# Kernel optimization log

Measured on AMD Instinct MI355X. Metric: run time of the kernel, lower is better.

The kernel has to match this reference:

```python
import jax, jax.numpy as jnp
import numpy as np

D_MODEL = 1024
N_HEADS = 16
HEAD_DIM = D_MODEL // N_HEADS


def setup_inputs() -> dict:
    key = jax.random.key(0)
    k_x, k_qkv, k_out = jax.random.split(key, 3)
    x = jax.random.normal(k_x, (4, 2048, D_MODEL), dtype=jnp.float32)
    # nn.Linear weights are (out_features, in_features); init std=0.02
    w_qkv = jax.random.normal(k_qkv, (3 * D_MODEL, D_MODEL), dtype=jnp.float32) * 0.02
    w_out = jax.random.normal(k_out, (D_MODEL, D_MODEL), dtype=jnp.float32) * 0.02
    return {"x": x, "w_qkv": w_qkv, "w_out": w_out}


def reference(x, w_qkv, w_out):
    B, T, C = x.shape
    H, Dh = N_HEADS, HEAD_DIM
    # qkv projection: x @ w_qkv.T -> (B, T, 3C)
    qkv = jnp.einsum('btc,oc->bto', x, w_qkv)
    q, k, v = jnp.split(qkv, 3, axis=-1)

    def split_heads(t):
        return t.reshape(B, T, H, Dh).transpose(0, 2, 1, 3)  # (B, H, T, Dh)

    q, k, v = split_heads(q), split_heads(k), split_heads(v)
    scale = jnp.sqrt(jnp.asarray(Dh, dtype=x.dtype))
    scores = jnp.einsum('bhqd,bhkd->bhqk', q, k) / scale  # (B, H, T, T)
    causal = jnp.tril(jnp.ones((T, T), dtype=bool))
    scores = jnp.where(causal[None, None], scores, jnp.asarray(-jnp.inf, dtype=scores.dtype))
    attn = jax.nn.softmax(scores, axis=-1)
    out = jnp.einsum('bhqk,bhkd->bhqd', attn, v)  # (B, H, T, Dh)
    out = out.transpose(0, 2, 1, 3).reshape(B, T, C)
    return jnp.einsum('btc,oc->bto', out, w_out)
```

## Files before the change

kernel.cpp:

```cpp
#include <hip/hip_runtime.h>

typedef __attribute__((ext_vector_type(8))) short bf16x8;
typedef __attribute__((ext_vector_type(4))) float f32x4;
typedef __attribute__((ext_vector_type(16))) float f32x16;
typedef __attribute__((ext_vector_type(4))) int i32x4;
using u16 = unsigned short;

constexpr int Bsz = 4, T = 2048, C = 1024, H = 16, Dh = 64;
constexpr int Mrows = Bsz * T;
constexpr int K_DIM = 1024;
constexpr float QSCALE = 0.18033688011112042f;

__device__ inline u16 f2bf(float f) {
    unsigned u = __builtin_bit_cast(unsigned, f);
    u += 0x7FFFu + ((u >> 16) & 1u);
    return (u16)(u >> 16);
}

__device__ inline void g2l16(const void* g, void* l) {
    __builtin_amdgcn_global_load_lds((const __attribute__((address_space(1))) void*)g,
                                     (__attribute__((address_space(3))) void*)l, 16, 0, 0);
}

__device__ inline unsigned pk2(float lo, float hi) {
    unsigned d;
    asm("v_cvt_pk_bf16_f32 %0, %1, %2" : "=v"(d) : "v"(lo), "v"(hi));
    return d;
}
__device__ inline void swap32(unsigned& a, unsigned& b) {
    asm("v_permlane32_swap_b32 %0, %1" : "+v"(a), "+v"(b));
}

__global__ __launch_bounds__(256)
void cvt_k(const float* __restrict__ x, const float* __restrict__ wq,
           const float* __restrict__ wo, u16* __restrict__ xb,
           u16* __restrict__ wqb, u16* __restrict__ wob)
{
    int idx = blockIdx.x * 256 + threadIdx.x;
    const float* src; u16* dst; int rel;
    if (idx < 1048576)      { src = x;  dst = xb;  rel = idx; }
    else if (idx < 1441792) { src = wq; dst = wqb; rel = idx - 1048576; }
    else                    { src = wo; dst = wob; rel = idx - 1441792; }
    size_t off = (size_t)rel * 8;
    float4 a = *(const float4*)(src + off);
    float4 b = *(const float4*)(src + off + 4);
    unsigned r0 = (unsigned)f2bf(a.x) | ((unsigned)f2bf(a.y) << 16);
    unsigned r1 = (unsigned)f2bf(a.z) | ((unsigned)f2bf(a.w) << 16);
    unsigned r2 = (unsigned)f2bf(b.x) | ((unsigned)f2bf(b.y) << 16);
    unsigned r3 = (unsigned)f2bf(b.z) | ((unsigned)f2bf(b.w) << 16);
    *(uint4*)(dst + off) = make_uint4(r0, r1, r2, r3);
}

__device__ inline void stage_g(u16* lds, const u16* gb, int ldg, int tid) {
    #pragma unroll
    for (int i = 0; i < 4; ++i) {
        int ch = i * 256 + tid;
        int r = ch >> 3, c8 = ch & 7;
        int sc = c8 ^ (r & 7);
        g2l16(gb + (size_t)r * ldg + sc * 8, lds + (i * 256 + (tid & 192)) * 8);
    }
}

template<int MODE>
__global__ __launch_bounds__(256)
void gemm_k(const u16* __restrict__ Ab, const u16* __restrict__ Bb,
            float* __restrict__ Op, u16* __restrict__ qws,
            u16* __restrict__ kws, u16* __restrict__ vtws)
{
    __shared__ alignas(16) u16 As[128 * 64];
    __shared__ alignas(16) u16 Bs[128 * 64];
    const int tid = threadIdx.x;
    const int l = tid & 63, wid = tid >> 6;
    const int wm = wid >> 1, wn = wid & 1;
    const int lane16 = l & 15, lhi = l >> 4;
    const int m0 = blockIdx.x * 128;
    const int n0 = (MODE == 2 ? 2 * C : 0) + blockIdx.y * 128;

    const u16* Abase = Ab + (size_t)m0 * K_DIM;
    const u16* Bbase = Bb + (size_t)n0 * K_DIM;

    f32x4 acc[4][4] = {};

    for (int ks = 0; ks < K_DIM / 64; ++ks) {
        __syncthreads();
        stage_g(As, Abase + ks * 64, K_DIM, tid);
        stage_g(Bs, Bbase + ks * 64, K_DIM, tid);
        __syncthreads();
        #pragma unroll
        for (int kc = 0; kc < 2; kc++) {
            bf16x8 af[4], bfr[4];
            #pragma unroll
            for (int mi = 0; mi < 4; mi++) {
                int row = wm * 64 + mi * 16 + lane16;
                int byte = row * 128 + kc * 64 + lhi * 16; byte ^= (row & 7) << 4;
                af[mi] = *(const bf16x8*)((const char*)As + byte);
            }
            #pragma unroll
            for (int ni = 0; ni < 4; ni++) {
                int row = wn * 64 + ni * 16 + lane16;
                int byte = row * 128 + kc * 64 + lhi * 16; byte ^= (row & 7) << 4;
                bfr[ni] = *(const bf16x8*)((const char*)Bs + byte);
            }
            #pragma unroll
            for (int mi = 0; mi < 4; mi++)
                #pragma unroll
                for (int ni = 0; ni < 4; ni++) {
                    if constexpr (MODE == 2)
                        acc[mi][ni] = __builtin_amdgcn_mfma_f32_16x16x32_bf16(
                            bfr[ni], af[mi], acc[mi][ni], 0, 0, 0);
                    else
                        acc[mi][ni] = __builtin_amdgcn_mfma_f32_16x16x32_bf16(
                            af[mi], bfr[ni], acc[mi][ni], 0, 0, 0);
                }
        }
    }

    if constexpr (MODE == 2) {
        #pragma unroll
        for (int mi = 0; mi < 4; mi++)
            #pragma unroll
            for (int ni = 0; ni < 4; ni++)
                #pragma unroll
                for (int r = 0; r < 4; r++) {
                    int wr = n0 + wn * 64 + ni * 16 + lhi * 4 + r;
                    int tg = m0 + wm * 64 + mi * 16 + lane16;
                    int hh = (wr >> 6) & 15, d = wr & 63;
                    int bb = tg >> 11, tt = tg & 2047;
                    size_t off = (((size_t)bb * H + hh) * Dh + d) * T + tt;
                    vtws[off] = f2bf(acc[mi][ni][r]);
                }
    } else {
        #pragma unroll
        for (int mi = 0; mi < 4; mi++)
            #pragma unroll
            for (int ni = 0; ni < 4; ni++)
                #pragma unroll
                for (int r = 0; r < 4; r++) {
                    int gm = m0 + wm * 64 + mi * 16 + lhi * 4 + r;
                    int gn = n0 + wn * 64 + ni * 16 + lane16;
                    float val = acc[mi][ni][r];
                    if constexpr (MODE == 0) {
                        int hh = (gn >> 6) & 15, d = gn & 63;
                        int bb = gm >> 11, t = gm & 2047;
                        size_t off = (((size_t)bb * H + hh) * T + t) * Dh + d;
                        if (gn < C) qws[off] = f2bf(val * QSCALE);
                        else        kws[off] = f2bf(val);
                    } else {
                        Op[(size_t)gm * C + gn] = val;
                    }
                }
    }
}

__device__ inline bf16x8 ldsfrag(const u16* base, int row, int cc) {
    int byte = (row << 7) + (cc << 4); byte ^= (row & 7) << 4;
    return *(const bf16x8*)((const char*)base + byte);
}

__device__ inline void stage_t(u16* lds, const u16* gb, int rstride, int tid) {
    #pragma unroll
    for (int it = 0; it < 2; ++it) {
        int chunk = it * 256 + tid;
        int r = chunk >> 3, cc = chunk & 7;
        int sc = cc ^ (r & 7);
        g2l16(gb + (size_t)r * rstride + sc * 8, lds + (it * 256 + (tid & 192)) * 8);
    }
}

__global__ __launch_bounds__(256, 2)
void attn_k(const u16* __restrict__ qws, const u16* __restrict__ kws,
            const u16* __restrict__ vtws, u16* __restrict__ ows)
{
    __shared__ alignas(16) u16 KL[2][64 * 64];
    __shared__ alignas(16) u16 VL[2][64 * 64];

    const int bid = blockIdx.x;
    const int qt   = (bid < 256) ? 7 - (bid & 7) : (bid & 7);
    const int head = ((bid < 256) ? 0 : 32) + ((bid & 255) >> 3);
    const int b = head >> 4, h = head & 15;
    const int tid = threadIdx.x, w = tid >> 6, l = tid & 63;
    const int l31 = l & 31, hi = l >> 5;

    const size_t hoff = (size_t)head * (T * Dh);
    const u16* Qg  = qws + hoff;
    const u16* Kg  = kws + hoff;
    const u16* Vtg = vtws + hoff;

    const int qb_w = qt * 256 + w * 64;
    const int nt = 4 * qt + 4;

    bf16x8 qf[2][4];
    #pragma unroll
    for (int q2 = 0; q2 < 2; ++q2)
        #pragma unroll
        for (int c = 0; c < 4; ++c)
            qf[q2][c] = *(const bf16x8*)(Qg + (size_t)(qb_w + q2 * 32 + l31) * Dh
                                         + c * 16 + hi * 8);

    f32x16 o[2][2] = {};
    float mrun[2] = {-__builtin_inff(), -__builtin_inff()};
    float lrun[2] = {0.f, 0.f};

    stage_t(KL[0], Kg, Dh, tid);
    stage_t(VL[0], Vtg, T, tid);
    __syncthreads();

    for (int t = 0; t < nt; ++t) {
        const int cur = t & 1;
        if (t + 1 < nt) {
            stage_t(KL[cur ^ 1], Kg + (size_t)(t + 1) * 64 * Dh, Dh, tid);
            stage_t(VL[cur ^ 1], Vtg + (t + 1) * 64, T, tid);
        }
        const int kv0 = t * 64;
        if (kv0 <= qb_w + 63) {
            const u16* Kb = KL[cur];
            const u16* Vb = VL[cur];

            bf16x8 kf[2][4];
            #pragma unroll
            for (int kvh = 0; kvh < 2; ++kvh)
                #pragma unroll
                for (int c = 0; c < 4; ++c)
                    kf[kvh][c] = ldsfrag(Kb, kvh * 32 + l31, c * 2 + hi);

            unsigned paf[2][4][4];
            const bool act0 = kv0 <= qb_w + 31;

            #pragma unroll
            for (int q2 = 0; q2 < 2; ++q2) {
                if (q2 == 0 && !act0) continue;
                f32x16 s0{}, s1{};
                #pragma unroll
                for (int c = 0; c < 4; ++c) {
                    s0 = __builtin_amdgcn_mfma_f32_32x32x16_bf16(kf[0][c], qf[q2][c], s0, 0, 0, 0);
                    s1 = __builtin_amdgcn_mfma_f32_32x32x16_bf16(kf[1][c], qf[q2][c], s1, 0, 0, 0);
                }
                const int qbb = qb_w + q2 * 32;
                if (kv0 + 63 > qbb) {
                    int qg = qbb + l31;
                    #pragma unroll
                    for (int r = 0; r < 16; ++r) {
                        int kvg = kv0 + (r & 3) + 8 * (r >> 2) + 4 * hi;
                        if (kvg > qg)      s0[r] = -__builtin_inff();
                        if (kvg + 32 > qg) s1[r] = -__builtin_inff();
                    }
                }
                float pmax = s0[0];
                #pragma unroll
                for (int r = 1; r < 16; ++r) pmax = fmaxf(pmax, s0[r]);
                #pragma unroll
                for (int r = 0; r < 16; ++r) pmax = fmaxf(pmax, s1[r]);
                pmax = fmaxf(pmax, __shfl_xor(pmax, 32));

                if (!__all(pmax - mrun[q2] <= 8.0f)) {
                    float mn = fmaxf(mrun[q2], pmax);
                    float corr = __builtin_amdgcn_exp2f(mrun[q2] - mn);
                    mrun[q2] = mn;
                    lrun[q2] *= corr;
                    #pragma unroll
                    for (int r = 0; r < 16; ++r) {
                        float cr = __shfl(corr, (r & 3) + 8 * (r >> 2) + 4 * hi);
                        o[q2][0][r] *= cr;
                        o[q2][1][r] *= cr;
                    }
                }
                float p0[16], p1[16];
                #pragma unroll
                for (int r = 0; r < 16; ++r) {
                    p0[r] = __builtin_amdgcn_exp2f(s0[r] - mrun[q2]);
                    p1[r] = __builtin_amdgcn_exp2f(s1[r] - mrun[q2]);
                    lrun[q2] += p0[r] + p1[r];
                }
                unsigned cc[8];
                #pragma unroll
                for (int i = 0; i < 4; ++i) cc[i]     = pk2(p0[2 * i], p0[2 * i + 1]);
                #pragma unroll
                for (int i = 0; i < 4; ++i) cc[4 + i] = pk2(p0[8 + 2 * i], p0[9 + 2 * i]);
                swap32(cc[0], cc[2]); swap32(cc[1], cc[3]);
                swap32(cc[4], cc[6]); swap32(cc[5], cc[7]);
                #pragma unroll
                for (int i = 0; i < 4; ++i) { paf[q2][0][i] = cc[i]; paf[q2][1][i] = cc[4 + i]; }
                #pragma unroll
                for (int i = 0; i < 4; ++i) cc[i]     = pk2(p1[2 * i], p1[2 * i + 1]);
                #pragma unroll
                for (int i = 0; i < 4; ++i) cc[4 + i] = pk2(p1[8 + 2 * i], p1[9 + 2 * i]);
                swap32(cc[0], cc[2]); swap32(cc[1], cc[3]);
                swap32(cc[4], cc[6]); swap32(cc[5], cc[7]);
                #pragma unroll
                for (int i = 0; i < 4; ++i) { paf[q2][2][i] = cc[i]; paf[q2][3][i] = cc[4 + i]; }
            }

            bf16x8 vf[2][4];
            #pragma unroll
            for (int db = 0; db < 2; ++db)
                #pragma unroll
                for (int kb = 0; kb < 4; ++kb)
                    vf[db][kb] = ldsfrag(Vb, db * 32 + l31, kb * 2 + hi);

            #pragma unroll
            for (int q2 = 0; q2 < 2; ++q2) {
                if (q2 == 0 && !act0) continue;
                #pragma unroll
                for (int db = 0; db < 2; ++db)
                    #pragma unroll
                    for (int kb = 0; kb < 4; ++kb) {
                        i32x4 wv = {(int)paf[q2][kb][0], (int)paf[q2][kb][1],
                                    (int)paf[q2][kb][2], (int)paf[q2][kb][3]};
                        o[q2][db] = __builtin_amdgcn_mfma_f32_32x32x16_bf16(
                            __builtin_bit_cast(bf16x8, wv), vf[db][kb], o[q2][db], 0, 0, 0);
                    }
            }
        }
        __syncthreads();
    }

    #pragma unroll
    for (int q2 = 0; q2 < 2; ++q2) {
        float lt = lrun[q2] + __shfl_xor(lrun[q2], 32);
        float inv = 1.0f / lt;
        int qbb = qb_w + q2 * 32;
        #pragma unroll
        for (int r = 0; r < 16; ++r) {
            int cr = (r & 3) + 8 * (r >> 2) + 4 * hi;
            float il = __shfl(inv, cr);
            size_t rowoff = ((size_t)b * T + qbb + cr) * C + h * Dh + l31;
            ows[rowoff]      = f2bf(o[q2][0][r] * il);
            ows[rowoff + 32] = f2bf(o[q2][1][r] * il);
        }
    }
}

extern "C" void kernel_launch(void* const* d_in, const int* in_sizes, int n_in,
                              void* d_out, int out_size, void* d_ws, size_t ws_size,
                              hipStream_t stream)
{
    const float* x     = (const float*)d_in[0];
    const float* w_qkv = (const float*)d_in[1];
    const float* w_out = (const float*)d_in[2];
    float* out = (float*)d_out;

    const size_t SZ = (size_t)Bsz * H * T * Dh;
    u16* qws   = (u16*)d_ws;
    u16* kws   = qws + SZ;
    u16* vtws  = kws + SZ;
    u16* xb    = vtws + SZ;
    u16* ows   = xb;
    u16* wqkvb = xb + SZ;
    u16* woutb = wqkvb + (size_t)3 * C * C;

    cvt_k<<<dim3(6144), 256, 0, stream>>>(x, w_qkv, w_out, xb, wqkvb, woutb);

    dim3 gqk(Mrows / 128, (2 * C) / 128);
    gemm_k<0><<<gqk, 256, 0, stream>>>(xb, wqkvb, nullptr, qws, kws, vtws);
    dim3 gv(Mrows / 128, C / 128);
    gemm_k<2><<<gv, 256, 0, stream>>>(xb, wqkvb, nullptr, qws, kws, vtws);

    attn_k<<<dim3(512), 256, 0, stream>>>(qws, kws, vtws, ows);

    dim3 g1(Mrows / 128, C / 128);
    gemm_k<1><<<g1, 256, 0, stream>>>(ows, woutb, out, nullptr, nullptr, nullptr);
}
```

Measured before the change: 175.4 us.

## Rebalance causal attention by pairing light and heavy 128-row query tiles per block

```diff
diff --git a/kernel.cpp b/kernel.cpp
--- a/kernel.cpp
+++ b/kernel.cpp
@@ -175,8 +175,8 @@
     __shared__ alignas(16) u16 VL[2][64 * 64];
 
     const int bid = blockIdx.x;
-    const int qt   = (bid < 256) ? 7 - (bid & 7) : (bid & 7);
-    const int head = ((bid < 256) ? 0 : 32) + ((bid & 255) >> 3);
+    const int p = bid & 7;
+    const int head = bid >> 3;
     const int b = head >> 4, h = head & 15;
     const int tid = threadIdx.x, w = tid >> 6, l = tid & 63;
     const int l31 = l & 31, hi = l >> 5;
@@ -186,58 +186,52 @@
     const u16* Kg  = kws + hoff;
     const u16* Vtg = vtws + hoff;
 
-    const int qb_w = qt * 256 + w * 64;
-    const int nt = 4 * qt + 4;
-
-    bf16x8 qf[2][4];
     #pragma unroll
-    for (int q2 = 0; q2 < 2; ++q2)
+    for (int half = 0; half < 2; ++half) {
+        const int qt = half ? 15 - p : p;
+        const int qb = qt * 128;
+        const int nt = 2 * qt + 2;
+        const int qbw = qb + w * 32;
+
+        bf16x8 qf[4];
         #pragma unroll
         for (int c = 0; c < 4; ++c)
-            qf[q2][c] = *(const bf16x8*)(Qg + (size_t)(qb_w + q2 * 32 + l31) * Dh
-                                         + c * 16 + hi * 8);
-
-    f32x16 o[2][2] = {};
-    float mrun[2] = {-__builtin_inff(), -__builtin_inff()};
-    float lrun[2] = {0.f, 0.f};
-
-    stage_t(KL[0], Kg, Dh, tid);
-    stage_t(VL[0], Vtg, T, tid);
-    __syncthreads();
-
-    for (int t = 0; t < nt; ++t) {
-        const int cur = t & 1;
-        if (t + 1 < nt) {
-            stage_t(KL[cur ^ 1], Kg + (size_t)(t + 1) * 64 * Dh, Dh, tid);
-            stage_t(VL[cur ^ 1], Vtg + (t + 1) * 64, T, tid);
-        }
-        const int kv0 = t * 64;
-        if (kv0 <= qb_w + 63) {
-            const u16* Kb = KL[cur];
-            const u16* Vb = VL[cur];
-
-            bf16x8 kf[2][4];
-            #pragma unroll
-            for (int kvh = 0; kvh < 2; ++kvh)
-                #pragma unroll
-                for (int c = 0; c < 4; ++c)
-                    kf[kvh][c] = ldsfrag(Kb, kvh * 32 + l31, c * 2 + hi);
-
-            unsigned paf[2][4][4];
-            const bool act0 = kv0 <= qb_w + 31;
-
-            #pragma unroll
-            for (int q2 = 0; q2 < 2; ++q2) {
-                if (q2 == 0 && !act0) continue;
+            qf[c] = *(const bf16x8*)(Qg + (size_t)(qbw + l31) * Dh + c * 16 + hi * 8);
+
+        f32x16 o0{}, o1{};
+        float mrun = -__builtin_inff(), lrun = 0.f;
+
+        stage_t(KL[0], Kg, Dh, tid);
+        stage_t(VL[0], Vtg, T, tid);
+        __syncthreads();
+
+        for (int t = 0; t < nt; ++t) {
+            const int cur = t & 1;
+            if (t + 1 < nt) {
+                stage_t(KL[cur ^ 1], Kg + (size_t)(t + 1) * 64 * Dh, Dh, tid);
+                stage_t(VL[cur ^ 1], Vtg + (t + 1) * 64, T, tid);
+            }
+            const int kv0 = t * 64;
+            if (kv0 <= qbw + 31) {
+                const u16* Kb = KL[cur];
+                const u16* Vb = VL[cur];
+
+                bf16x8 kf0[4], kf1[4];
+                #pragma unroll
+                for (int c = 0; c < 4; ++c) {
+                    kf0[c] = ldsfrag(Kb, l31, c * 2 + hi);
+                    kf1[c] = ldsfrag(Kb, 32 + l31, c * 2 + hi);
+                }
+
                 f32x16 s0{}, s1{};
                 #pragma unroll
                 for (int c = 0; c < 4; ++c) {
-                    s0 = __builtin_amdgcn_mfma_f32_32x32x16_bf16(kf[0][c], qf[q2][c], s0, 0, 0, 0);
-                    s1 = __builtin_amdgcn_mfma_f32_32x32x16_bf16(kf[1][c], qf[q2][c], s1, 0, 0, 0);
-                }
-                const int qbb = qb_w + q2 * 32;
-                if (kv0 + 63 > qbb) {
-                    int qg = qbb + l31;
+                    s0 = __builtin_amdgcn_mfma_f32_32x32x16_bf16(kf0[c], qf[c], s0, 0, 0, 0);
+                    s1 = __builtin_amdgcn_mfma_f32_32x32x16_bf16(kf1[c], qf[c], s1, 0, 0, 0);
+                }
+
+                if (kv0 + 63 > qbw) {
+                    int qg = qbw + l31;
                     #pragma unroll
                     for (int r = 0; r < 16; ++r) {
                         int kvg = kv0 + (r & 3) + 8 * (r >> 2) + 4 * hi;
@@ -245,32 +239,41 @@
                         if (kvg + 32 > qg) s1[r] = -__builtin_inff();
                     }
                 }
-                float pmax = s0[0];
-                #pragma unroll
-                for (int r = 1; r < 16; ++r) pmax = fmaxf(pmax, s0[r]);
-                #pragma unroll
-                for (int r = 0; r < 16; ++r) pmax = fmaxf(pmax, s1[r]);
-                pmax = fmaxf(pmax, __shfl_xor(pmax, 32));
-
-                if (!__all(pmax - mrun[q2] <= 8.0f)) {
-                    float mn = fmaxf(mrun[q2], pmax);
-                    float corr = __builtin_amdgcn_exp2f(mrun[q2] - mn);
-                    mrun[q2] = mn;
-                    lrun[q2] *= corr;
+
+                float m16[16];
+                #pragma unroll
+                for (int r = 0; r < 16; ++r) m16[r] = fmaxf(s0[r], s1[r]);
+                #pragma unroll
+                for (int d = 8; d; d >>= 1)
+                    #pragma unroll
+                    for (int r = 0; r < d; ++r) m16[r] = fmaxf(m16[r], m16[r + d]);
+                float pmax = fmaxf(m16[0], __shfl_xor(m16[0], 32));
+
+                if (!__all(pmax - mrun <= 8.0f)) {
+                    float mn = fmaxf(mrun, pmax);
+                    float corr = __builtin_amdgcn_exp2f(mrun - mn);
+                    mrun = mn;
+                    lrun *= corr;
                     #pragma unroll
                     for (int r = 0; r < 16; ++r) {
                         float cr = __shfl(corr, (r & 3) + 8 * (r >> 2) + 4 * hi);
-                        o[q2][0][r] *= cr;
-                        o[q2][1][r] *= cr;
+                        o0[r] *= cr;
+                        o1[r] *= cr;
                     }
                 }
                 float p0[16], p1[16];
+                float t0 = 0.f, t1 = 0.f, t2 = 0.f, t3 = 0.f;
                 #pragma unroll
                 for (int r = 0; r < 16; ++r) {
-                    p0[r] = __builtin_amdgcn_exp2f(s0[r] - mrun[q2]);
-                    p1[r] = __builtin_amdgcn_exp2f(s1[r] - mrun[q2]);
-                    lrun[q2] += p0[r] + p1[r];
-                }
+                    p0[r] = __builtin_amdgcn_exp2f(s0[r] - mrun);
+                    p1[r] = __builtin_amdgcn_exp2f(s1[r] - mrun);
+                    float s = p0[r] + p1[r];
+                    if ((r & 3) == 0) t0 += s; else if ((r & 3) == 1) t1 += s;
+                    else if ((r & 3) == 2) t2 += s; else t3 += s;
+                }
+                lrun += (t0 + t1) + (t2 + t3);
+
+                unsigned paf[4][4];
                 unsigned cc[8];
                 #pragma unroll
                 for (int i = 0; i < 4; ++i) cc[i]     = pk2(p0[2 * i], p0[2 * i + 1]);
@@ -279,7 +282,7 @@
                 swap32(cc[0], cc[2]); swap32(cc[1], cc[3]);
                 swap32(cc[4], cc[6]); swap32(cc[5], cc[7]);
                 #pragma unroll
-                for (int i = 0; i < 4; ++i) { paf[q2][0][i] = cc[i]; paf[q2][1][i] = cc[4 + i]; }
+                for (int i = 0; i < 4; ++i) { paf[0][i] = cc[i]; paf[1][i] = cc[4 + i]; }
                 #pragma unroll
                 for (int i = 0; i < 4; ++i) cc[i]     = pk2(p1[2 * i], p1[2 * i + 1]);
                 #pragma unroll
@@ -287,45 +290,31 @@
                 swap32(cc[0], cc[2]); swap32(cc[1], cc[3]);
                 swap32(cc[4], cc[6]); swap32(cc[5], cc[7]);
                 #pragma unroll
-                for (int i = 0; i < 4; ++i) { paf[q2][2][i] = cc[i]; paf[q2][3][i] = cc[4 + i]; }
+                for (int i = 0; i < 4; ++i) { paf[2][i] = cc[i]; paf[3][i] = cc[4 + i]; }
+
+                #pragma unroll
+                for (int kb = 0; kb < 4; ++kb) {
+                    i32x4 wv = {(int)paf[kb][0], (int)paf[kb][1],
+                                (int)paf[kb][2], (int)paf[kb][3]};
+                    bf16x8 pa = __builtin_bit_cast(bf16x8, wv);
+                    bf16x8 v0 = ldsfrag(Vb, l31,      kb * 2 + hi);
+                    bf16x8 v1 = ldsfrag(Vb, 32 + l31, kb * 2 + hi);
+                    o0 = __builtin_amdgcn_mfma_f32_32x32x16_bf16(pa, v0, o0, 0, 0, 0);
+                    o1 = __builtin_amdgcn_mfma_f32_32x32x16_bf16(pa, v1, o1, 0, 0, 0);
+                }
             }
-
-            bf16x8 vf[2][4];
-            #pragma unroll
-            for (int db = 0; db < 2; ++db)
-                #pragma unroll
-                for (int kb = 0; kb < 4; ++kb)
-                    vf[db][kb] = ldsfrag(Vb, db * 32 + l31, kb * 2 + hi);
-
-            #pragma unroll
-            for (int q2 = 0; q2 < 2; ++q2) {
-                if (q2 == 0 && !act0) continue;
-                #pragma unroll
-                for (int db = 0; db < 2; ++db)
-                    #pragma unroll
-                    for (int kb = 0; kb < 4; ++kb) {
-                        i32x4 wv = {(int)paf[q2][kb][0], (int)paf[q2][kb][1],
-                                    (int)paf[q2][kb][2], (int)paf[q2][kb][3]};
-                        o[q2][db] = __builtin_amdgcn_mfma_f32_32x32x16_bf16(
-                            __builtin_bit_cast(bf16x8, wv), vf[db][kb], o[q2][db], 0, 0, 0);
-                    }
-            }
+            __syncthreads();
         }
-        __syncthreads();
-    }
-
-    #pragma unroll
-    for (int q2 = 0; q2 < 2; ++q2) {
-        float lt = lrun[q2] + __shfl_xor(lrun[q2], 32);
+
+        float lt = lrun + __shfl_xor(lrun, 32);
         float inv = 1.0f / lt;
-        int qbb = qb_w + q2 * 32;
         #pragma unroll
         for (int r = 0; r < 16; ++r) {
             int cr = (r & 3) + 8 * (r >> 2) + 4 * hi;
             float il = __shfl(inv, cr);
-            size_t rowoff = ((size_t)b * T + qbb + cr) * C + h * Dh + l31;
-            ows[rowoff]      = f2bf(o[q2][0][r] * il);
-            ows[rowoff + 32] = f2bf(o[q2][1][r] * il);
+            size_t rowoff = ((size_t)b * T + qb + w * 32 + cr) * C + h * Dh + l31;
+            ows[rowoff]      = f2bf(o0[r] * il);
+            ows[rowoff + 32] = f2bf(o1[r] * il);
         }
     }
 }
```

Result: faster. 167.4 us (-4.6%).
